# Performance work log

Hardware: AMD Instinct MI355X
Metric: run time of the kernel (lower is better)

Reference implementation:

```python
import jax, jax.numpy as jnp
import numpy as np

B, S, D, H = 2, 2048, 1024, 16
DK = D // H


def setup_inputs() -> dict:
    key = jax.random.key(0)
    ks = jax.random.split(key, 13)
    scale = 1.0 / np.sqrt(D)
    return {
        "query": jax.random.normal(ks[0], (B, S, D), jnp.float32),
        "key": jax.random.normal(ks[1], (B, S, D), jnp.float32),
        "value": jax.random.normal(ks[2], (B, S, D), jnp.float32),
        "mask": jax.random.randint(ks[3], (B, S, S), 0, 2, jnp.int32),
        "Wq": jax.random.normal(ks[4], (D, D), jnp.float32) * scale,
        "bq": jnp.zeros((D,), jnp.float32),
        "Wk": jax.random.normal(ks[5], (D, D), jnp.float32) * scale,
        "bk": jnp.zeros((D,), jnp.float32),
        "Wv": jax.random.normal(ks[6], (D, D), jnp.float32) * scale,
        "bv": jnp.zeros((D,), jnp.float32),
        "Wo": jax.random.normal(ks[7], (D, D), jnp.float32) * scale,
        "bo": jnp.zeros((D,), jnp.float32),
    }


def _split_heads(x):
    # [B,S,D] -> [B,H,S,DK]
    b, s, _ = x.shape
    return x.reshape(b, s, H, DK).transpose(0, 2, 1, 3)


def reference(query, key, value, mask, Wq, bq, Wk, bk, Wv, bv, Wo, bo):
    q = _split_heads(query @ Wq + bq)
    k = _split_heads(key @ Wk + bk)
    v = _split_heads(value @ Wv + bv)
    # scaled dot-product scores [B,H,Sq,Sk]
    scores = jnp.einsum("bhqd,bhkd->bhqk", q, k) / jnp.sqrt(jnp.float32(DK))
    scores = jnp.where(mask[:, None, :, :] == 0, jnp.float32(-1e9), scores)
    p_attn = jax.nn.softmax(scores, axis=-1)  # dropout p=0.0 -> identity
    x = jnp.einsum("bhqk,bhkd->bhqd", p_attn, v)
    x = x.transpose(0, 2, 1, 3).reshape(query.shape[0], -1, D)
    return x @ Wo + bo
```

## Files before the change

### kernel.cpp

```cpp
#include <hip/hip_runtime.h>
#include <cstdint>

#define B_ 2
#define S_ 2048
#define D_ 1024
#define H_ 16
#define DK_ 64
#define SCALE_ 0.18033688011112042f

typedef float f32x4 __attribute__((ext_vector_type(4)));
typedef float f32x16 __attribute__((ext_vector_type(16)));
typedef __bf16 bf16x8 __attribute__((ext_vector_type(8)));
typedef unsigned short u16x8 __attribute__((ext_vector_type(8)));
typedef unsigned short u16x4 __attribute__((ext_vector_type(4)));
typedef unsigned int u32x4 __attribute__((ext_vector_type(4)));

__device__ __forceinline__ unsigned short f2bf(float x) {
  unsigned int u = __builtin_bit_cast(unsigned int, x);
  u += 0x7FFFu + ((u >> 16) & 1u);
  return (unsigned short)(u >> 16);
}

__device__ __forceinline__ void gload16(const void* g, void* l) {
  __builtin_amdgcn_global_load_lds((__attribute__((address_space(1))) void*)(void*)g,
                                   (__attribute__((address_space(3))) void*)l, 16, 0, 0);
}

__device__ __forceinline__ float exp2v(float x) {
  float r;
  asm("v_exp_f32 %0, %1" : "=v"(r) : "v"(x));
  return r;
}

__device__ __forceinline__ unsigned int cvtpk(float a, float b) {
  unsigned int r;
  asm("v_cvt_pk_bf16_f32 %0, %1, %2" : "=v"(r) : "v"(a), "v"(b));
  return r;
}

__device__ __forceinline__ unsigned int bit_mask(unsigned int w, int bit) {
#if __has_builtin(__builtin_amdgcn_sbfe)
  return (unsigned int)__builtin_amdgcn_sbfe((int)w, bit, 1);
#else
  return (unsigned int)((int)(w << (31 - bit)) >> 31);
#endif
}

__global__ __launch_bounds__(256) void prep_kernel(
    const float* __restrict__ q, const float* __restrict__ k, const float* __restrict__ v,
    unsigned short* __restrict__ oq, unsigned short* __restrict__ ok,
    unsigned short* __restrict__ ov,
    const float* __restrict__ w0, const float* __restrict__ w1,
    const float* __restrict__ w2, const float* __restrict__ w3,
    unsigned short* o0, unsigned short* o1, unsigned short* o2, unsigned short* o3,
    const int* __restrict__ mask, unsigned int* __restrict__ mb) {
  __shared__ float t[32][33];
  const int bid = blockIdx.x;
  const int tid = threadIdx.x;
  if (bid < 6144) {
    const int z = bid >> 11, vb = bid & 2047;
    const float* in = z == 0 ? q : z == 1 ? k : v;
    unsigned short* out = z == 0 ? oq : z == 1 ? ok : ov;
    const int n = B_ * S_ * D_;
    int idx = vb * 256 + tid;
#pragma unroll
    for (int i = idx * 4; i < n; i += 2048 * 256 * 4) {
      f32x4 vv = *(const f32x4*)(in + i);
      u16x4 o;
#pragma unroll
      for (int j = 0; j < 4; ++j) o[j] = f2bf(vv[j]);
      *(u16x4*)(out + i) = o;
    }
  } else if (bid < 10240) {
    const int r = bid - 6144;
    const int z = r >> 10, rr = r & 1023;
    const float* W;
    unsigned short* O;
    float sc = 1.f;
    if (z == 0) { W = w0; O = o0; sc = SCALE_; }
    else if (z == 1) { W = w1; O = o1; }
    else if (z == 2) { W = w2; O = o2; }
    else { W = w3; O = o3; }
    const int n0 = (rr & 31) * 32, k0 = (rr >> 5) * 32;
    const int tx = tid & 31, ty = tid >> 5;
    for (int i = ty; i < 32; i += 8) t[i][tx] = W[(size_t)(k0 + i) * D_ + n0 + tx];
    __syncthreads();
    for (int i = ty; i < 32; i += 8) O[(size_t)(n0 + i) * D_ + k0 + tx] = f2bf(t[tx][i] * sc);
  } else {
    const int wid = ((bid - 10240) << 2) + (tid >> 6);
    const int lane = tid & 63;
    size_t base = (size_t)wid << 6;
    unsigned long long bits = __ballot(mask[base + lane] != 0);
    if (lane == 0) *(unsigned long long*)(mb + (base >> 5)) = bits;
  }
}

template <int MODE>
__device__ __forceinline__ void gemm128(const unsigned short* __restrict__ A,
                                        const unsigned short* __restrict__ BT,
                                        const float* __restrict__ bias, float bsc,
                                        void* __restrict__ Cp, int M, int N, int K) {
  __shared__ unsigned short Al[128 * 32];
  __shared__ unsigned short Bl[128 * 32];
  const int tid = threadIdx.x;
  const int lane = tid & 63;
  const int w = tid >> 6;
  const int wr = w >> 1, wc = w & 1;
  const int wg = blockIdx.x + gridDim.x * blockIdx.y;
  const int work = (wg & 7) * 32 + (wg >> 3);
  const int nx = N >> 7;
  const int m0 = (work / nx) * 128, n0 = (work % nx) * 128;

  f32x4 acc[4][4] = {};
  const int nk = K / 32;
  const int srow = lane >> 2;
  const int scol = (lane & 3) * 8;

  const int fr = lane & 15;
  const int fc = (lane >> 4) * 8;

  for (int kt = 0; kt < nk; ++kt) {
    __syncthreads();
#pragma unroll
    for (int it = 0; it < 2; ++it) {
      int chunk = it * 4 + w;
      const unsigned short* ga = A + (size_t)(m0 + chunk * 16 + srow) * K + kt * 32 + scol;
      gload16(ga, &Al[chunk * 512]);
      const unsigned short* gb = BT + (size_t)(n0 + chunk * 16 + srow) * K + kt * 32 + scol;
      gload16(gb, &Bl[chunk * 512]);
    }
    __syncthreads();
    bf16x8 af[4], bf[4];
#pragma unroll
    for (int i = 0; i < 4; ++i)
      af[i] = __builtin_bit_cast(bf16x8, *(const u16x8*)&Al[(wr * 64 + i * 16 + fr) * 32 + fc]);
#pragma unroll
    for (int j = 0; j < 4; ++j)
      bf[j] = __builtin_bit_cast(bf16x8, *(const u16x8*)&Bl[(wc * 64 + j * 16 + fr) * 32 + fc]);
    __builtin_amdgcn_s_setprio(1);
#pragma unroll
    for (int i = 0; i < 4; ++i)
#pragma unroll
      for (int j = 0; j < 4; ++j)
        acc[i][j] = __builtin_amdgcn_mfma_f32_16x16x32_bf16(af[i], bf[j], acc[i][j], 0, 0, 0);
    __builtin_amdgcn_s_setprio(0);
  }

  const int rg = (lane >> 4) * 4;
  const int cg = lane & 15;
#pragma unroll
  for (int i = 0; i < 4; ++i)
#pragma unroll
    for (int j = 0; j < 4; ++j) {
      int col = n0 + wc * 64 + j * 16 + cg;
      float bv = bias[col] * bsc;
#pragma unroll
      for (int e = 0; e < 4; ++e) {
        int row = m0 + wr * 64 + i * 16 + rg + e;
        float v = acc[i][j][e] + bv;
        if (MODE == 1)
          ((float*)Cp)[(size_t)row * N + col] = v;
        else if (MODE == 0)
          ((unsigned short*)Cp)[(size_t)row * N + col] = f2bf(v);
        else
          ((unsigned short*)Cp)[((size_t)(row >> 11) * D_ + col) * S_ + (row & (S_ - 1))] = f2bf(v);
      }
    }
}

__global__ __launch_bounds__(256) void qkv_gemm_kernel(
    const unsigned short* __restrict__ xq, const unsigned short* __restrict__ xk,
    const unsigned short* __restrict__ xv, const unsigned short* __restrict__ wtq,
    const unsigned short* __restrict__ wtk, const unsigned short* __restrict__ wtv,
    const float* __restrict__ bq, const float* __restrict__ bk, const float* __restrict__ bv,
    unsigned short* q, unsigned short* k, unsigned short* vt) {
  if (blockIdx.z == 0)
    gemm128<0>(xq, wtq, bq, SCALE_, (void*)q, B_ * S_, D_, D_);
  else if (blockIdx.z == 1)
    gemm128<0>(xk, wtk, bk, 1.f, (void*)k, B_ * S_, D_, D_);
  else
    gemm128<2>(xv, wtv, bv, 1.f, (void*)vt, B_ * S_, D_, D_);
}

__global__ __launch_bounds__(256) void out_gemm_kernel(const unsigned short* __restrict__ x,
                                                       const unsigned short* __restrict__ wto,
                                                       const float* __restrict__ bo,
                                                       float* __restrict__ out) {
  gemm128<1>(x, wto, bo, 1.f, (void*)out, B_ * S_, D_, D_);
}

__global__ __launch_bounds__(256) void attn_kernel(const unsigned short* __restrict__ Q,
                                                   const unsigned short* __restrict__ K,
                                                   const unsigned short* __restrict__ Vt,
                                                   const unsigned int* __restrict__ mb,
                                                   unsigned short* __restrict__ X) {
  __shared__ unsigned short Kl[2][128 * 64];
  __shared__ unsigned short Vl[2][2][64 * 64];

  const int tid = threadIdx.x;
  const int lane = tid & 63;
  const int w = tid >> 6;
  const int ql = lane & 31;
  const int hi = lane >> 5;

  const int wg = blockIdx.x + gridDim.x * blockIdx.y;
  const int swz = (wg & 7) * 64 + (wg >> 3);
  const int qt = swz & 15;
  const int bh = swz >> 4;
  const int b = bh >> 4, h = bh & 15;
  const int q_g = qt * 128 + w * 32 + ql;

  const size_t qkbase = ((size_t)b * S_) * D_ + h * DK_;
  const size_t vtbase = ((size_t)b * D_ + h * DK_) * S_;

  bf16x8 qf[4];
  {
    const unsigned short* qp = Q + qkbase + (size_t)q_g * D_ + hi * 8;
#pragma unroll
    for (int c = 0; c < 4; ++c)
      qf[c] = __builtin_bit_cast(bf16x8, *(const u16x8*)(qp + c * 16));
  }

  const int lr = lane >> 3;
  const int seg = (lane & 7) ^ lr;
  const unsigned short* Ks = K + qkbase + (size_t)(w * 32 + lr) * D_ + seg * 8;
  const unsigned short* Vs = Vt + vtbase + (size_t)(w * 16 + lr) * S_ + seg * 8;

  auto stage = [&](int kt, int bufi) {
#pragma unroll
    for (int c = 0; c < 4; ++c)
      gload16(Ks + ((size_t)kt * 128 + c * 8) * D_, &Kl[bufi][(w * 32 + c * 8) * 64]);
#pragma unroll
    for (int c = 0; c < 4; ++c)
      gload16(Vs + (size_t)((c & 1) * 8) * S_ + kt * 128 + (c >> 1) * 64,
              &Vl[bufi][c >> 1][(w * 16 + (c & 1) * 8) * 64]);
  };

  const unsigned long long* mrow =
      (const unsigned long long*)mb + ((size_t)b * S_ + q_g) * 32;

  f32x16 o0 = {}, o1 = {};
  f32x16 o2 = {};
  const int sw = (ql & 7) << 4;

  const unsigned int one2 = 0x3F803F80u;
  const bf16x8 onesf = __builtin_bit_cast(bf16x8, u32x4{one2, one2, one2, one2});

  stage(0, 0);
  const int NT = S_ / 128;

  for (int kt = 0; kt < NT; ++kt) {
    const int buf = kt & 1;
    __syncthreads();
    if (kt < NT - 1) stage(kt + 1, buf ^ 1);
    unsigned long long M0 = mrow[kt * 2], M1 = mrow[kt * 2 + 1];

#pragma unroll
    for (int hh = 0; hh < 2; ++hh) {
      const unsigned long long M = hh ? M1 : M0;
      const char* Kb = (const char*)&Kl[buf][hh * 64 * 64];

      f32x16 s0 = {}, s1 = {};
      __builtin_amdgcn_s_setprio(1);
#pragma unroll
      for (int c = 0; c < 4; ++c) {
        int col = c * 32 + hi * 16;
        bf16x8 k0 = __builtin_bit_cast(bf16x8, *(const u16x8*)(Kb + ((ql * 128 + col) ^ sw)));
        s0 = __builtin_amdgcn_mfma_f32_32x32x16_bf16(k0, qf[c], s0, 0, 0, 0);
        bf16x8 k1 = __builtin_bit_cast(bf16x8, *(const u16x8*)(Kb + (((32 + ql) * 128 + col) ^ sw)));
        s1 = __builtin_amdgcn_mfma_f32_32x32x16_bf16(k1, qf[c], s1, 0, 0, 0);
      }
      __builtin_amdgcn_s_setprio(0);

      unsigned int W0 = (unsigned int)(M >> (hi * 4));
      unsigned int W1 = (unsigned int)(M >> (32 + hi * 4));
#pragma unroll
      for (int r = 0; r < 16; ++r) {
        const int krl = (r & 3) + 8 * (r >> 2);
        unsigned int mk0 = bit_mask(W0, krl);
        float p0 = exp2v(s0[r]);
        s0[r] = __builtin_bit_cast(float, __builtin_bit_cast(unsigned int, p0) & mk0);
        unsigned int mk1 = bit_mask(W1, krl);
        float p1 = exp2v(s1[r]);
        s1[r] = __builtin_bit_cast(float, __builtin_bit_cast(unsigned int, p1) & mk1);
      }

      u32x4 pw[4];
#pragma unroll
      for (int kc = 0; kc < 4; ++kc) {
        const int rb = (kc & 1) * 8;
        float pa0, pa1, pa2, pa3, pa4, pa5, pa6, pa7;
        if (kc < 2) {
          pa0 = s0[rb + 0]; pa1 = s0[rb + 1]; pa2 = s0[rb + 2]; pa3 = s0[rb + 3];
          pa4 = s0[rb + 4]; pa5 = s0[rb + 5]; pa6 = s0[rb + 6]; pa7 = s0[rb + 7];
        } else {
          pa0 = s1[rb + 0]; pa1 = s1[rb + 1]; pa2 = s1[rb + 2]; pa3 = s1[rb + 3];
          pa4 = s1[rb + 4]; pa5 = s1[rb + 5]; pa6 = s1[rb + 6]; pa7 = s1[rb + 7];
        }
        unsigned int w0 = cvtpk(pa0, pa1), w1 = cvtpk(pa2, pa3);
        unsigned int w2 = cvtpk(pa4, pa5), w3 = cvtpk(pa6, pa7);
        unsigned int u0, u1, u2, u3;
#if __has_builtin(__builtin_amdgcn_permlane32_swap)
        { auto r02 = __builtin_amdgcn_permlane32_swap(w0, w2, false, false);
          u0 = r02[0]; u2 = r02[1]; }
        { auto r13 = __builtin_amdgcn_permlane32_swap(w1, w3, false, false);
          u1 = r13[0]; u3 = r13[1]; }
#else
        { unsigned int t0 = (unsigned int)__shfl_xor((int)w0, 32);
          unsigned int t2 = (unsigned int)__shfl_xor((int)w2, 32);
          u0 = hi ? t2 : w0; u2 = hi ? w2 : t0;
          unsigned int t1 = (unsigned int)__shfl_xor((int)w1, 32);
          unsigned int t3 = (unsigned int)__shfl_xor((int)w3, 32);
          u1 = hi ? t3 : w1; u3 = hi ? w3 : t1; }
#endif
        pw[kc] = u32x4{u0, u1, u2, u3};
      }

      const char* Vb = (const char*)&Vl[buf][hh][0];
      __builtin_amdgcn_s_setprio(1);
#pragma unroll
      for (int kc = 0; kc < 4; ++kc) {
        bf16x8 pf = __builtin_bit_cast(bf16x8, pw[kc]);
        int col = kc * 32 + hi * 16;
        bf16x8 v0 = __builtin_bit_cast(bf16x8, *(const u16x8*)(Vb + ((ql * 128 + col) ^ sw)));
        o0 = __builtin_amdgcn_mfma_f32_32x32x16_bf16(v0, pf, o0, 0, 0, 0);
        bf16x8 v1 = __builtin_bit_cast(bf16x8, *(const u16x8*)(Vb + (((32 + ql) * 128 + col) ^ sw)));
        o1 = __builtin_amdgcn_mfma_f32_32x32x16_bf16(v1, pf, o1, 0, 0, 0);
        o2 = __builtin_amdgcn_mfma_f32_32x32x16_bf16(onesf, pf, o2, 0, 0, 0);
      }
      __builtin_amdgcn_s_setprio(0);
    }
  }

  float inv = 1.f / o2[0];
  unsigned short* Xp = X + ((size_t)b * S_ + q_g) * D_ + h * DK_;
#pragma unroll
  for (int rb = 0; rb < 4; ++rb) {
    int d0 = 8 * rb + 4 * hi;
    *(unsigned int*)(Xp + d0) = cvtpk(o0[4 * rb + 0] * inv, o0[4 * rb + 1] * inv);
    *(unsigned int*)(Xp + d0 + 2) = cvtpk(o0[4 * rb + 2] * inv, o0[4 * rb + 3] * inv);
    *(unsigned int*)(Xp + 32 + d0) = cvtpk(o1[4 * rb + 0] * inv, o1[4 * rb + 1] * inv);
    *(unsigned int*)(Xp + 32 + d0 + 2) = cvtpk(o1[4 * rb + 2] * inv, o1[4 * rb + 3] * inv);
  }
}

extern "C" void kernel_launch(void* const* d_in, const int* in_sizes, int n_in,
                              void* d_out, int out_size, void* d_ws, size_t ws_size,
                              hipStream_t stream) {
  const float* query = (const float*)d_in[0];
  const float* key = (const float*)d_in[1];
  const float* value = (const float*)d_in[2];
  const int* mask = (const int*)d_in[3];
  const float* Wq = (const float*)d_in[4];
  const float* bq = (const float*)d_in[5];
  const float* Wk = (const float*)d_in[6];
  const float* bk = (const float*)d_in[7];
  const float* Wv = (const float*)d_in[8];
  const float* bv = (const float*)d_in[9];
  const float* Wo = (const float*)d_in[10];
  const float* bo = (const float*)d_in[11];
  float* out = (float*)d_out;

  const size_t ACT = (size_t)B_ * S_ * D_;
  const size_t WSZ = (size_t)D_ * D_;
  unsigned short* ws = (unsigned short*)d_ws;
  unsigned short* xq = ws;
  unsigned short* xk = xq + ACT;
  unsigned short* xv = xk + ACT;
  unsigned short* wtq = xv + ACT;
  unsigned short* wtk = wtq + WSZ;
  unsigned short* wtv = wtk + WSZ;
  unsigned short* wto = wtv + WSZ;
  unsigned short* qb = wto + WSZ;
  unsigned short* kb = qb + ACT;
  unsigned short* vt = kb + ACT;
  unsigned int* mbp = (unsigned int*)(vt + ACT);
  unsigned short* xb = xq;

  prep_kernel<<<43008, 256, 0, stream>>>(query, key, value, xq, xk, xv,
                                         Wq, Wk, Wv, Wo, wtq, wtk, wtv, wto,
                                         mask, mbp);

  dim3 gg(8, 32, 3);
  qkv_gemm_kernel<<<gg, 256, 0, stream>>>(xq, xk, xv, wtq, wtk, wtv, bq, bk, bv, qb, kb, vt);

  dim3 ag(S_ / 128, B_ * H_);
  attn_kernel<<<ag, 256, 0, stream>>>(qb, kb, vt, mbp, xb);

  dim3 og(8, 32, 1);
  out_gemm_kernel<<<og, 256, 0, stream>>>(xb, wto, bo, out);
}
```

Baseline: 169.4 us.

## Restructure attention loop to batch LDS loads and MFMAs across both halves

```diff
diff --git a/kernel.cpp b/kernel.cpp
--- a/kernel.cpp
+++ b/kernel.cpp
@@ -189,11 +189,11 @@
   gemm128<1>(x, wto, bo, 1.f, (void*)out, B_ * S_, D_, D_);
 }
 
-__global__ __launch_bounds__(256) void attn_kernel(const unsigned short* __restrict__ Q,
-                                                   const unsigned short* __restrict__ K,
-                                                   const unsigned short* __restrict__ Vt,
-                                                   const unsigned int* __restrict__ mb,
-                                                   unsigned short* __restrict__ X) {
+__global__ __launch_bounds__(256, 2) void attn_kernel(const unsigned short* __restrict__ Q,
+                                                      const unsigned short* __restrict__ K,
+                                                      const unsigned short* __restrict__ Vt,
+                                                      const unsigned int* __restrict__ mb,
+                                                      unsigned short* __restrict__ X) {
   __shared__ unsigned short Kl[2][128 * 64];
   __shared__ unsigned short Vl[2][2][64 * 64];
 
@@ -252,53 +252,68 @@
   for (int kt = 0; kt < NT; ++kt) {
     const int buf = kt & 1;
     __syncthreads();
+    unsigned long long M0 = mrow[kt * 2], M1 = mrow[kt * 2 + 1];
+
+    bf16x8 kf[2][2][4];
+#pragma unroll
+    for (int hh = 0; hh < 2; ++hh) {
+      const char* Kb = (const char*)&Kl[buf][hh * 64 * 64];
+#pragma unroll
+      for (int r = 0; r < 2; ++r)
+#pragma unroll
+        for (int c = 0; c < 4; ++c)
+          kf[hh][r][c] = __builtin_bit_cast(
+              bf16x8, *(const u16x8*)(Kb + (((r * 32 + ql) * 128 + c * 32 + hi * 16) ^ sw)));
+    }
     if (kt < NT - 1) stage(kt + 1, buf ^ 1);
-    unsigned long long M0 = mrow[kt * 2], M1 = mrow[kt * 2 + 1];
-
+
+    f32x16 s[2][2] = {};
+    __builtin_amdgcn_s_setprio(1);
+#pragma unroll
+    for (int hh = 0; hh < 2; ++hh)
+#pragma unroll
+      for (int c = 0; c < 4; ++c) {
+        s[hh][0] = __builtin_amdgcn_mfma_f32_32x32x16_bf16(kf[hh][0][c], qf[c], s[hh][0], 0, 0, 0);
+        s[hh][1] = __builtin_amdgcn_mfma_f32_32x32x16_bf16(kf[hh][1][c], qf[c], s[hh][1], 0, 0, 0);
+      }
+    __builtin_amdgcn_s_setprio(0);
+
+    bf16x8 vf[2][2][4];
+#pragma unroll
+    for (int hh = 0; hh < 2; ++hh) {
+      const char* Vb = (const char*)&Vl[buf][hh][0];
+#pragma unroll
+      for (int nt = 0; nt < 2; ++nt)
+#pragma unroll
+        for (int kc = 0; kc < 4; ++kc)
+          vf[hh][nt][kc] = __builtin_bit_cast(
+              bf16x8, *(const u16x8*)(Vb + (((nt * 32 + ql) * 128 + kc * 32 + hi * 16) ^ sw)));
+    }
+
+    u32x4 pw[2][4];
 #pragma unroll
     for (int hh = 0; hh < 2; ++hh) {
       const unsigned long long M = hh ? M1 : M0;
-      const char* Kb = (const char*)&Kl[buf][hh * 64 * 64];
-
-      f32x16 s0 = {}, s1 = {};
-      __builtin_amdgcn_s_setprio(1);
-#pragma unroll
-      for (int c = 0; c < 4; ++c) {
-        int col = c * 32 + hi * 16;
-        bf16x8 k0 = __builtin_bit_cast(bf16x8, *(const u16x8*)(Kb + ((ql * 128 + col) ^ sw)));
-        s0 = __builtin_amdgcn_mfma_f32_32x32x16_bf16(k0, qf[c], s0, 0, 0, 0);
-        bf16x8 k1 = __builtin_bit_cast(bf16x8, *(const u16x8*)(Kb + (((32 + ql) * 128 + col) ^ sw)));
-        s1 = __builtin_amdgcn_mfma_f32_32x32x16_bf16(k1, qf[c], s1, 0, 0, 0);
-      }
-      __builtin_amdgcn_s_setprio(0);
-
       unsigned int W0 = (unsigned int)(M >> (hi * 4));
       unsigned int W1 = (unsigned int)(M >> (32 + hi * 4));
 #pragma unroll
       for (int r = 0; r < 16; ++r) {
         const int krl = (r & 3) + 8 * (r >> 2);
         unsigned int mk0 = bit_mask(W0, krl);
-        float p0 = exp2v(s0[r]);
-        s0[r] = __builtin_bit_cast(float, __builtin_bit_cast(unsigned int, p0) & mk0);
+        float p0 = exp2v(s[hh][0][r]);
+        s[hh][0][r] = __builtin_bit_cast(float, __builtin_bit_cast(unsigned int, p0) & mk0);
         unsigned int mk1 = bit_mask(W1, krl);
-        float p1 = exp2v(s1[r]);
-        s1[r] = __builtin_bit_cast(float, __builtin_bit_cast(unsigned int, p1) & mk1);
+        float p1 = exp2v(s[hh][1][r]);
+        s[hh][1][r] = __builtin_bit_cast(float, __builtin_bit_cast(unsigned int, p1) & mk1);
       }
-
-      u32x4 pw[4];
 #pragma unroll
       for (int kc = 0; kc < 4; ++kc) {
         const int rb = (kc & 1) * 8;
-        float pa0, pa1, pa2, pa3, pa4, pa5, pa6, pa7;
-        if (kc < 2) {
-          pa0 = s0[rb + 0]; pa1 = s0[rb + 1]; pa2 = s0[rb + 2]; pa3 = s0[rb + 3];
-          pa4 = s0[rb + 4]; pa5 = s0[rb + 5]; pa6 = s0[rb + 6]; pa7 = s0[rb + 7];
-        } else {
-          pa0 = s1[rb + 0]; pa1 = s1[rb + 1]; pa2 = s1[rb + 2]; pa3 = s1[rb + 3];
-          pa4 = s1[rb + 4]; pa5 = s1[rb + 5]; pa6 = s1[rb + 6]; pa7 = s1[rb + 7];
-        }
-        unsigned int w0 = cvtpk(pa0, pa1), w1 = cvtpk(pa2, pa3);
-        unsigned int w2 = cvtpk(pa4, pa5), w3 = cvtpk(pa6, pa7);
+        const int st = kc >> 1;
+        unsigned int w0 = cvtpk(s[hh][st][rb + 0], s[hh][st][rb + 1]);
+        unsigned int w1 = cvtpk(s[hh][st][rb + 2], s[hh][st][rb + 3]);
+        unsigned int w2 = cvtpk(s[hh][st][rb + 4], s[hh][st][rb + 5]);
+        unsigned int w3 = cvtpk(s[hh][st][rb + 6], s[hh][st][rb + 7]);
         unsigned int u0, u1, u2, u3;
 #if __has_builtin(__builtin_amdgcn_permlane32_swap)
         { auto r02 = __builtin_amdgcn_permlane32_swap(w0, w2, false, false);
@@ -313,23 +328,21 @@
           unsigned int t3 = (unsigned int)__shfl_xor((int)w3, 32);
           u1 = hi ? t3 : w1; u3 = hi ? w3 : t1; }
 #endif
-        pw[kc] = u32x4{u0, u1, u2, u3};
+        pw[hh][kc] = u32x4{u0, u1, u2, u3};
       }
-
-      const char* Vb = (const char*)&Vl[buf][hh][0];
-      __builtin_amdgcn_s_setprio(1);
+    }
+
+    __builtin_amdgcn_s_setprio(1);
+#pragma unroll
+    for (int hh = 0; hh < 2; ++hh)
 #pragma unroll
       for (int kc = 0; kc < 4; ++kc) {
-        bf16x8 pf = __builtin_bit_cast(bf16x8, pw[kc]);
-        int col = kc * 32 + hi * 16;
-        bf16x8 v0 = __builtin_bit_cast(bf16x8, *(const u16x8*)(Vb + ((ql * 128 + col) ^ sw)));
-        o0 = __builtin_amdgcn_mfma_f32_32x32x16_bf16(v0, pf, o0, 0, 0, 0);
-        bf16x8 v1 = __builtin_bit_cast(bf16x8, *(const u16x8*)(Vb + (((32 + ql) * 128 + col) ^ sw)));
-        o1 = __builtin_amdgcn_mfma_f32_32x32x16_bf16(v1, pf, o1, 0, 0, 0);
+        bf16x8 pf = __builtin_bit_cast(bf16x8, pw[hh][kc]);
+        o0 = __builtin_amdgcn_mfma_f32_32x32x16_bf16(vf[hh][0][kc], pf, o0, 0, 0, 0);
+        o1 = __builtin_amdgcn_mfma_f32_32x32x16_bf16(vf[hh][1][kc], pf, o1, 0, 0, 0);
         o2 = __builtin_amdgcn_mfma_f32_32x32x16_bf16(onesf, pf, o2, 0, 0, 0);
       }
-      __builtin_amdgcn_s_setprio(0);
-    }
+    __builtin_amdgcn_s_setprio(0);
   }
 
   float inv = 1.f / o2[0];
```

Measured after the change: 163.6 us. -3.4%, faster.
